# Performance work log

Measured on AMD Instinct MI355X. Metric: run time of the kernel, lower is better.

The kernel has to match this reference:

```python
import jax, jax.numpy as jnp
import numpy as np

# Dimensions (see shape_source): 192x192 images, 10 MC samples, 4 classes (3 fg), batch 16
B, S, CLS, H, W = 16, 10, 4, 192, 192
FG = CLS - 1
FSCALE = 3   # neighbor-count kernel
CSCALE = 3   # constraint-reward kernel
K = float(CSCALE * CSCALE)


def setup_inputs() -> dict:
    key = jax.random.key(0)
    k1, k2 = jax.random.split(key)
    logits = jax.random.normal(k1, (B, CLS, H, W), dtype=jnp.float32)
    preds = jax.nn.softmax(logits, axis=1)          # per-pixel class probabilities
    samples = jax.random.randint(k2, (B, S, H, W), 0, CLS, dtype=jnp.int32)  # sampled label maps
    return {"preds": preds, "samples": samples}


def _conv_ones(x, ksize):
    # x: [N, H, W]; all-ones ksize x ksize conv, SAME padding (== pad (k-1)/2 in torch)
    kern = jnp.ones((1, 1, ksize, ksize), x.dtype)
    y = jax.lax.conv_general_dilated(x[:, None], kern, (1, 1), 'SAME')
    return y[:, 0]


def _dilate8(m):
    # 3x3 max-pool == one step of 8-connectivity dilation (skimage full connectivity)
    return jax.lax.reduce_window(m, 0.0, jax.lax.max, (3, 3), (1, 1), 'SAME')


def _flood(fg, seed):
    # connected component of fg containing flat index `seed` (8-connectivity),
    # equivalent to skimage.flood_fill from the seed followed by == new_value
    m0 = jnp.zeros(fg.size, fg.dtype).at[seed].set(1.0).reshape(fg.shape) * fg
    def cond(st):
        return st[1]
    def body(st):
        m, _ = st
        d = _dilate8(m) * fg
        return d, jnp.any(d != m)
    m, _ = jax.lax.while_loop(cond, body, (m0, jnp.array(True)))
    return m


def _connectivity_rewards(samples):
    # samples: [B, S, H, W] int class maps -> rewards [B, S, H, W]
    cls_ids = jnp.arange(1, CLS)
    fg = (samples[:, :, None] == cls_ids[None, None, :, None, None]).astype(jnp.float32)  # [B,S,FG,H,W]
    fgf = fg.reshape(-1, H, W)                     # [B*S*FG, H, W]
    nb = _conv_ones(fgf, FSCALE) * fgf             # foreground neighbor counts
    seeds = jnp.argmax(nb.reshape(nb.shape[0], -1), axis=1)  # seed = max-neighbor pixel (first max)
    comp = jax.vmap(_flood)(fgf, seeds)            # largest-seeded connected component
    fc = _conv_ones(comp, CSCALE) * comp           # F_fg_neigbors
    reward = fc / K                                # soft reward
    per_c = reward - (fgf - comp)                  # + isolation penalty: -(fg - fill_connect)
    return per_c.reshape(B, S, FG, H, W).sum(axis=2)


def reference(preds, samples):
    rewards = _connectivity_rewards(samples)       # [B,S,H,W], constant wrt preds
    # prob of the sampled class at each pixel: preds[b, samples[b,s,h,w], h, w]
    probs = jnp.take_along_axis(
        jnp.broadcast_to(preds[:, None], (B, S, CLS, H, W)),
        samples[:, :, None].astype(jnp.int32), axis=2)[:, :, 0]
    # REINFORCE-style constraint loss: maximize reward-weighted log-prob
    loss = -(jnp.log(probs + 1e-8) * rewards).mean()
    return loss
```

## Files before the change

kernel.cpp:

```cpp
#include <hip/hip_runtime.h>
#include <stdint.h>

#define BB 16
#define SS 10
#define CLSN 4
#define FGN 3
#define HH 192
#define WW 192
#define NPIX (HH * WW)
#define WPR 3
#define NWORDS (HH * WPR)
#define NPAIR (BB * SS)
#define NTASK (NPAIR * FGN)
#define NT 256
#define NW 4

typedef unsigned long long u64;
typedef unsigned short u16;

#define FAD(a, b, c, s, cy)            \
    do {                               \
        u64 t_ = (a) ^ (b);            \
        (s) = t_ ^ (c);                \
        (cy) = ((a) & (b)) | (t_ & (c)); \
    } while (0)

#define SMEAR3(u0, u1, u2, s0, s1, s2)                          \
    do {                                                        \
        (s0) = (u0) | ((u0) << 1) | ((u0) >> 1) | ((u1) << 63); \
        (s1) = (u1) | ((u1) << 1) | ((u0) >> 63) | ((u1) >> 1) | ((u2) << 63); \
        (s2) = (u2) | ((u2) << 1) | ((u1) >> 63) | ((u2) >> 1); \
    } while (0)

__device__ __forceinline__ void plane9(const u64* bd, int k,
                                       u64& P0, u64& P1, u64& P2, u64& P3, u64& mid)
{
    const int r = k / WPR;
    const int wc = k - r * WPR;
    u64 rows[3][3];
#pragma unroll
    for (int di = 0; di < 3; ++di) {
        int rr = r + di - 1;
#pragma unroll
        for (int dj = 0; dj < 3; ++dj) {
            int ww = wc + dj - 1;
            rows[di][dj] = (rr >= 0 && rr < HH && ww >= 0 && ww < WPR)
                           ? bd[rr * WPR + ww] : 0ULL;
        }
    }
    mid = rows[1][1];
    u64 in[9];
#pragma unroll
    for (int i = 0; i < 3; ++i) {
        u64 m = rows[i][1], lf = rows[i][0], rg = rows[i][2];
        in[3 * i + 0] = m;
        in[3 * i + 1] = (m << 1) | (lf >> 63);
        in[3 * i + 2] = (m >> 1) | (rg << 63);
    }
    u64 s0a, c0a, s0b, c0b, s0c, c0c, c0d, s1a, c1a, c1b;
    FAD(in[0], in[1], in[2], s0a, c0a);
    FAD(in[3], in[4], in[5], s0b, c0b);
    FAD(in[6], in[7], in[8], s0c, c0c);
    FAD(s0a, s0b, s0c, P0, c0d);
    FAD(c0a, c0b, c0c, s1a, c1a);
    P1 = s1a ^ c0d;
    c1b = s1a & c0d;
    P2 = c1a ^ c1b;
    P3 = c1a & c1b;
}

__global__ __launch_bounds__(NT) void cc_fused(
    const float* __restrict__ preds,
    const int* __restrict__ samples,
    double* __restrict__ acc)
{
    __shared__ u64 fgw[NWORDS];
    __shared__ u64 cmp[NWORDS];
    __shared__ unsigned wkey[NW];
    __shared__ double wsum[NW];
    __shared__ unsigned seedSh;
    __shared__ int cntSh;
    __shared__ short wlist[NWORDS];

    const int blk = blockIdx.x;
    const int c = 1 + blk / NPAIR;
    const int pair = blk % NPAIR;
    const int b = pair / SS;

    const int tid  = threadIdx.x;
    const int lane = tid & 63;
    const int wv   = tid >> 6;

    const int* __restrict__ smp  = samples + (size_t)pair * NPIX;
    const float* __restrict__ pp = preds + ((size_t)b * CLSN + c) * NPIX;

    if (tid == 0) cntSh = 0;

    float facc = 0.0f;

    {
        u16* nib = (u16*)fgw;
        for (int sc = 0; sc < 9; ++sc) {
            const int ci = sc * NT + tid;
            const int px = ci << 4;
            const int4 v0 = *(const int4*)(smp + px);
            const int4 v1 = *(const int4*)(smp + px + 4);
            const int4 v2 = *(const int4*)(smp + px + 8);
            const int4 v3 = *(const int4*)(smp + px + 12);
            const float4 q0 = *(const float4*)(pp + px);
            const float4 q1 = *(const float4*)(pp + px + 4);
            const float4 q2 = *(const float4*)(pp + px + 8);
            const float4 q3 = *(const float4*)(pp + px + 12);
            unsigned m = 0u;
#define ACC1(vv, qq, sh)                                              \
            {                                                          \
                const bool hit_ = ((vv) == c);                         \
                m |= ((unsigned)hit_) << (sh);                         \
                facc -= hit_ ? __logf((qq) + 1e-8f) : 0.0f;            \
            }
            ACC1(v0.x, q0.x, 0)  ACC1(v0.y, q0.y, 1)
            ACC1(v0.z, q0.z, 2)  ACC1(v0.w, q0.w, 3)
            ACC1(v1.x, q1.x, 4)  ACC1(v1.y, q1.y, 5)
            ACC1(v1.z, q1.z, 6)  ACC1(v1.w, q1.w, 7)
            ACC1(v2.x, q2.x, 8)  ACC1(v2.y, q2.y, 9)
            ACC1(v2.z, q2.z, 10) ACC1(v2.w, q2.w, 11)
            ACC1(v3.x, q3.x, 12) ACC1(v3.y, q3.y, 13)
            ACC1(v3.z, q3.z, 14) ACC1(v3.w, q3.w, 15)
#undef ACC1
            nib[ci] = (u16)m;
        }
    }
    __syncthreads();

    {
        unsigned bestkey = 0u;
        for (int k = tid; k < NWORDS; k += NT) {
            u64 P0, P1, P2, P3, mid;
            plane9(fgw, k, P0, P1, P2, P3, mid);
            if (mid) {
                u64 cand = mid, t;
                unsigned v = 0;
                t = cand & P3; if (t) { cand = t; v |= 8u; }
                t = cand & P2; if (t) { cand = t; v |= 4u; }
                t = cand & P1; if (t) { cand = t; v |= 2u; }
                t = cand & P0; if (t) { cand = t; v |= 1u; }
                unsigned pix = ((unsigned)k << 6) + (unsigned)(__ffsll(cand) - 1);
                unsigned key = (v << 16) | (36863u - pix);
                if (key > bestkey) bestkey = key;
            }
        }
#pragma unroll
        for (int off = 32; off > 0; off >>= 1) {
            unsigned o = (unsigned)__shfl_xor((int)bestkey, off, 64);
            if (o > bestkey) bestkey = o;
        }
        if (lane == 0) wkey[wv] = bestkey;
    }
    __syncthreads();
    if (tid == 0) {
        unsigned kk = wkey[0];
        if (wkey[1] > kk) kk = wkey[1];
        if (wkey[2] > kk) kk = wkey[2];
        if (wkey[3] > kk) kk = wkey[3];
        seedSh = 36863u - (kk & 0xFFFFu);
    }
    __syncthreads();

    if (wv == 0) {
        const unsigned seed = seedSh;
        u64 f[3][3], cc[3][3];
        const int rbase = 3 * lane;
#pragma unroll
        for (int j = 0; j < 3; ++j)
#pragma unroll
            for (int w = 0; w < 3; ++w) {
                f[j][w] = fgw[(rbase + j) * WPR + w];
                cc[j][w] = 0ULL;
            }
        {
            const int sr = (int)(seed / WW), sw = ((int)seed % WW) >> 6, sb = (int)seed & 63;
            if (sr / 3 == lane)
                cc[sr % 3][sw] = (1ULL << sb) & f[sr % 3][sw];
        }
        for (;;) {
            u64 bA0 = __shfl_up(cc[2][0], 1, 64);
            u64 bA1 = __shfl_up(cc[2][1], 1, 64);
            u64 bA2 = __shfl_up(cc[2][2], 1, 64);
            u64 tB0 = __shfl_down(cc[0][0], 1, 64);
            u64 tB1 = __shfl_down(cc[0][1], 1, 64);
            u64 tB2 = __shfl_down(cc[0][2], 1, 64);
            if (lane == 0)  { bA0 = bA1 = bA2 = 0ULL; }
            if (lane == 63) { tB0 = tB1 = tB2 = 0ULL; }

            u64 o00 = cc[0][0], o01 = cc[0][1], o02 = cc[0][2];
            u64 o10 = cc[1][0], o11 = cc[1][1], o12 = cc[1][2];
            u64 o20 = cc[2][0], o21 = cc[2][1], o22 = cc[2][2];

#define RSTEP(A0, A1, A2, B0, B1, B2, C0, C1, C2, J)                          \
            {                                                                  \
                u64 u0 = (A0) | (B0) | (C0);                                   \
                u64 u1 = (A1) | (B1) | (C1);                                   \
                u64 u2 = (A2) | (B2) | (C2);                                   \
                u64 t0, t1, t2, s0, s1, s2;                                    \
                SMEAR3(u0, u1, u2, t0, t1, t2);                                \
                t0 &= f[J][0]; t1 &= f[J][1]; t2 &= f[J][2];                   \
                SMEAR3(t0, t1, t2, s0, s1, s2);                                \
                cc[J][0] = s0 & f[J][0];                                       \
                cc[J][1] = s1 & f[J][1];                                       \
                cc[J][2] = s2 & f[J][2];                                       \
            }
            RSTEP(bA0, bA1, bA2, cc[0][0], cc[0][1], cc[0][2], cc[1][0], cc[1][1], cc[1][2], 0)
            RSTEP(cc[0][0], cc[0][1], cc[0][2], cc[1][0], cc[1][1], cc[1][2], cc[2][0], cc[2][1], cc[2][2], 1)
            RSTEP(cc[1][0], cc[1][1], cc[1][2], cc[2][0], cc[2][1], cc[2][2], tB0, tB1, tB2, 2)
            RSTEP(cc[0][0], cc[0][1], cc[0][2], cc[1][0], cc[1][1], cc[1][2], cc[2][0], cc[2][1], cc[2][2], 1)
            RSTEP(bA0, bA1, bA2, cc[0][0], cc[0][1], cc[0][2], cc[1][0], cc[1][1], cc[1][2], 0)
#undef RSTEP

            u64 d = (cc[0][0] ^ o00) | (cc[0][1] ^ o01) | (cc[0][2] ^ o02)
                  | (cc[1][0] ^ o10) | (cc[1][1] ^ o11) | (cc[1][2] ^ o12)
                  | (cc[2][0] ^ o20) | (cc[2][1] ^ o21) | (cc[2][2] ^ o22);
            if (!__any(d != 0ULL)) break;
        }
#pragma unroll
        for (int j = 0; j < 3; ++j)
#pragma unroll
            for (int w = 0; w < 3; ++w)
                cmp[(rbase + j) * WPR + w] = cc[j][w];
    }
    __syncthreads();

    for (int k = tid; k < NWORDS; k += NT)
        if (cmp[k] != 0ULL) { int idx = atomicAdd(&cntSh, 1); wlist[idx] = (short)k; }
    __syncthreads();
    {
        const int n = cntSh;
        int i = wv;
        int kc = (i < n) ? (int)wlist[i] : -1;
        float pc = 0.0f;
        if (kc >= 0) pc = pp[(kc << 6) + lane];
        while (kc >= 0) {
            const int i2 = i + NW;
            const int k2 = (i2 < n) ? (int)wlist[i2] : -1;
            float p2 = 0.0f;
            if (k2 >= 0) p2 = pp[(k2 << 6) + lane];
            u64 P0, P1, P2, P3, mid;
            plane9(cmp, kc, P0, P1, P2, P3, mid);
            if ((mid >> lane) & 1ULL) {
                int ct = (int)((P0 >> lane) & 1ULL)
                       | ((int)((P1 >> lane) & 1ULL) << 1)
                       | ((int)((P2 >> lane) & 1ULL) << 2)
                       | ((int)((P3 >> lane) & 1ULL) << 3);
                facc += ((float)ct * (1.0f / 9.0f) + 1.0f) * __logf(pc + 1e-8f);
            }
            i = i2; kc = k2; pc = p2;
        }
    }

#pragma unroll
    for (int off = 32; off > 0; off >>= 1)
        facc += __shfl_xor(facc, off, 64);
    if (lane == 0) wsum[wv] = (double)facc;
    __syncthreads();
    if (tid == 0)
        atomicAdd(acc, wsum[0] + wsum[1] + wsum[2] + wsum[3]);
}

__global__ void finalize_kernel(const double* __restrict__ acc, float* __restrict__ out)
{
    if (threadIdx.x == 0 && blockIdx.x == 0)
        out[0] = (float)(-acc[0] / (double)((long long)BB * SS * NPIX));
}

extern "C" void kernel_launch(void* const* d_in, const int* in_sizes, int n_in,
                              void* d_out, int out_size, void* d_ws, size_t ws_size,
                              hipStream_t stream)
{
    const float* preds   = (const float*)d_in[0];
    const int*   samples = (const int*)d_in[1];
    double* acc = (double*)d_ws;

    hipMemsetAsync(acc, 0, sizeof(double), stream);
    hipLaunchKernelGGL(cc_fused, dim3(NTASK), dim3(NT), 0, stream,
                       preds, samples, acc);
    hipLaunchKernelGGL(finalize_kernel, dim3(1), dim3(64), 0, stream,
                       acc, (float*)d_out);
}
```

Baseline: 49.35 us.

## Flood fill with 8 rows per lane and a forward-backward row sweep

The single-wavefront bitmask flood fill now gives each of 24 active lanes 8 rows instead of giving each of 64 lanes 3 rows. Each iteration sweeps forward and backward over the 8 rows in registers, so information can travel up to 8 rows per iteration instead of 3. The change test is also folded into each step, and the per-row double smear is replaced by a single smear. The aim is fewer iterations of the shuffle-and-vote loop, in exchange for more serial work per lane and higher register pressure, with only 24 of 64 lanes doing useful work.

```diff
diff --git a/kernel.cpp b/kernel.cpp
--- a/kernel.cpp
+++ b/kernel.cpp
@@ -168,64 +168,74 @@
 
     if (wv == 0) {
         const unsigned seed = seedSh;
-        u64 f[3][3], cc[3][3];
-        const int rbase = 3 * lane;
-#pragma unroll
-        for (int j = 0; j < 3; ++j)
+        const bool act = lane < 24;
+        u64 f[8][3], cc[8][3];
+#pragma unroll
+        for (int j = 0; j < 8; ++j)
 #pragma unroll
             for (int w = 0; w < 3; ++w) {
-                f[j][w] = fgw[(rbase + j) * WPR + w];
+                const int k = (8 * lane + j) * WPR + w;
+                f[j][w] = act ? fgw[act ? k : 0] : 0ULL;
                 cc[j][w] = 0ULL;
             }
         {
-            const int sr = (int)(seed / WW), sw = ((int)seed % WW) >> 6, sb = (int)seed & 63;
-            if (sr / 3 == lane)
-                cc[sr % 3][sw] = (1ULL << sb) & f[sr % 3][sw];
+            const int sr = (int)(seed / WW), sc_ = (int)(seed % WW);
+            const int sw = sc_ >> 6, sb = sc_ & 63;
+            if ((sr >> 3) == lane) {
+                const int j = sr & 7;
+                u64 bit = (1ULL << sb);
+#pragma unroll
+                for (int jj = 0; jj < 8; ++jj)
+#pragma unroll
+                    for (int w = 0; w < 3; ++w)
+                        if (jj == j && w == sw) cc[jj][w] = bit & f[jj][w];
+            }
         }
         for (;;) {
-            u64 bA0 = __shfl_up(cc[2][0], 1, 64);
-            u64 bA1 = __shfl_up(cc[2][1], 1, 64);
-            u64 bA2 = __shfl_up(cc[2][2], 1, 64);
+            u64 bA0 = __shfl_up(cc[7][0], 1, 64);
+            u64 bA1 = __shfl_up(cc[7][1], 1, 64);
+            u64 bA2 = __shfl_up(cc[7][2], 1, 64);
             u64 tB0 = __shfl_down(cc[0][0], 1, 64);
             u64 tB1 = __shfl_down(cc[0][1], 1, 64);
             u64 tB2 = __shfl_down(cc[0][2], 1, 64);
-            if (lane == 0)  { bA0 = bA1 = bA2 = 0ULL; }
-            if (lane == 63) { tB0 = tB1 = tB2 = 0ULL; }
-
-            u64 o00 = cc[0][0], o01 = cc[0][1], o02 = cc[0][2];
-            u64 o10 = cc[1][0], o11 = cc[1][1], o12 = cc[1][2];
-            u64 o20 = cc[2][0], o21 = cc[2][1], o22 = cc[2][2];
-
-#define RSTEP(A0, A1, A2, B0, B1, B2, C0, C1, C2, J)                          \
+            if (lane == 0)   { bA0 = bA1 = bA2 = 0ULL; }
+            if (lane >= 23)  { tB0 = tB1 = tB2 = 0ULL; }
+
+            u64 d = 0ULL;
+#define FSTEP(J, T0, T1, T2, B0, B1, B2)                                      \
             {                                                                  \
-                u64 u0 = (A0) | (B0) | (C0);                                   \
-                u64 u1 = (A1) | (B1) | (C1);                                   \
-                u64 u2 = (A2) | (B2) | (C2);                                   \
-                u64 t0, t1, t2, s0, s1, s2;                                    \
-                SMEAR3(u0, u1, u2, t0, t1, t2);                                \
-                t0 &= f[J][0]; t1 &= f[J][1]; t2 &= f[J][2];                   \
-                SMEAR3(t0, t1, t2, s0, s1, s2);                                \
-                cc[J][0] = s0 & f[J][0];                                       \
-                cc[J][1] = s1 & f[J][1];                                       \
-                cc[J][2] = s2 & f[J][2];                                       \
-            }
-            RSTEP(bA0, bA1, bA2, cc[0][0], cc[0][1], cc[0][2], cc[1][0], cc[1][1], cc[1][2], 0)
-            RSTEP(cc[0][0], cc[0][1], cc[0][2], cc[1][0], cc[1][1], cc[1][2], cc[2][0], cc[2][1], cc[2][2], 1)
-            RSTEP(cc[1][0], cc[1][1], cc[1][2], cc[2][0], cc[2][1], cc[2][2], tB0, tB1, tB2, 2)
-            RSTEP(cc[0][0], cc[0][1], cc[0][2], cc[1][0], cc[1][1], cc[1][2], cc[2][0], cc[2][1], cc[2][2], 1)
-            RSTEP(bA0, bA1, bA2, cc[0][0], cc[0][1], cc[0][2], cc[1][0], cc[1][1], cc[1][2], 0)
-#undef RSTEP
-
-            u64 d = (cc[0][0] ^ o00) | (cc[0][1] ^ o01) | (cc[0][2] ^ o02)
-                  | (cc[1][0] ^ o10) | (cc[1][1] ^ o11) | (cc[1][2] ^ o12)
-                  | (cc[2][0] ^ o20) | (cc[2][1] ^ o21) | (cc[2][2] ^ o22);
+                u64 u0 = (T0) | cc[J][0] | (B0);                               \
+                u64 u1 = (T1) | cc[J][1] | (B1);                               \
+                u64 u2 = (T2) | cc[J][2] | (B2);                               \
+                u64 s0, s1, s2;                                                \
+                SMEAR3(u0, u1, u2, s0, s1, s2);                                \
+                s0 &= f[J][0]; s1 &= f[J][1]; s2 &= f[J][2];                   \
+                d |= (s0 & ~cc[J][0]) | (s1 & ~cc[J][1]) | (s2 & ~cc[J][2]);   \
+                cc[J][0] = s0; cc[J][1] = s1; cc[J][2] = s2;                   \
+            }
+            FSTEP(0, bA0, bA1, bA2, cc[1][0], cc[1][1], cc[1][2])
+            FSTEP(1, cc[0][0], cc[0][1], cc[0][2], cc[2][0], cc[2][1], cc[2][2])
+            FSTEP(2, cc[1][0], cc[1][1], cc[1][2], cc[3][0], cc[3][1], cc[3][2])
+            FSTEP(3, cc[2][0], cc[2][1], cc[2][2], cc[4][0], cc[4][1], cc[4][2])
+            FSTEP(4, cc[3][0], cc[3][1], cc[3][2], cc[5][0], cc[5][1], cc[5][2])
+            FSTEP(5, cc[4][0], cc[4][1], cc[4][2], cc[6][0], cc[6][1], cc[6][2])
+            FSTEP(6, cc[5][0], cc[5][1], cc[5][2], cc[7][0], cc[7][1], cc[7][2])
+            FSTEP(7, cc[6][0], cc[6][1], cc[6][2], tB0, tB1, tB2)
+            FSTEP(6, cc[5][0], cc[5][1], cc[5][2], cc[7][0], cc[7][1], cc[7][2])
+            FSTEP(5, cc[4][0], cc[4][1], cc[4][2], cc[6][0], cc[6][1], cc[6][2])
+            FSTEP(4, cc[3][0], cc[3][1], cc[3][2], cc[5][0], cc[5][1], cc[5][2])
+            FSTEP(3, cc[2][0], cc[2][1], cc[2][2], cc[4][0], cc[4][1], cc[4][2])
+            FSTEP(2, cc[1][0], cc[1][1], cc[1][2], cc[3][0], cc[3][1], cc[3][2])
+            FSTEP(1, cc[0][0], cc[0][1], cc[0][2], cc[2][0], cc[2][1], cc[2][2])
+            FSTEP(0, bA0, bA1, bA2, cc[1][0], cc[1][1], cc[1][2])
+#undef FSTEP
             if (!__any(d != 0ULL)) break;
         }
 #pragma unroll
-        for (int j = 0; j < 3; ++j)
+        for (int j = 0; j < 8; ++j)
 #pragma unroll
             for (int w = 0; w < 3; ++w)
-                cmp[(rbase + j) * WPR + w] = cc[j][w];
+                if (act) cmp[(8 * lane + j) * WPR + w] = cc[j][w];
     }
     __syncthreads();
 
```

After: 52.00 us. +5.4%, slower.

## Replace iterative bitmask flood fill with run-length union-find labeling

Applied to the files above, without the earlier changes.

Replaces the single-wave iterative dilation flood fill, whose iteration count grows with component diameter, with run-length encoding of each row, a prefix scan for run offsets, and a block-wide union-find over runs linked to overlapping runs in adjacent rows. Runs whose root matches the seed's run are written back to the component bitmask with atomicOr. This spreads the connectivity work across all 256 threads. In exchange it needs about 74 KB of dynamic shared memory per block, which lowers occupancy, and it adds shared-memory atomics. Runs beyond MAXRUNS are silently dropped.

```diff
diff --git a/kernel.cpp b/kernel.cpp
--- a/kernel.cpp
+++ b/kernel.cpp
@@ -14,22 +14,19 @@
 #define NTASK (NPAIR * FGN)
 #define NT 256
 #define NW 4
+#define MAXRUNS 8192
 
 typedef unsigned long long u64;
 typedef unsigned short u16;
+typedef unsigned int u32;
+
+#define SMEM_BYTES 75536
 
 #define FAD(a, b, c, s, cy)            \
     do {                               \
         u64 t_ = (a) ^ (b);            \
         (s) = t_ ^ (c);                \
         (cy) = ((a) & (b)) | (t_ & (c)); \
-    } while (0)
-
-#define SMEAR3(u0, u1, u2, s0, s1, s2)                          \
-    do {                                                        \
-        (s0) = (u0) | ((u0) << 1) | ((u0) >> 1) | ((u1) << 63); \
-        (s1) = (u1) | ((u1) << 1) | ((u0) >> 63) | ((u1) >> 1) | ((u2) << 63); \
-        (s2) = (u2) | ((u2) << 1) | ((u1) >> 63) | ((u2) >> 1); \
     } while (0)
 
 __device__ __forceinline__ void plane9(const u64* bd, int k,
@@ -69,17 +66,67 @@
     P3 = c1a & c1b;
 }
 
+__device__ __forceinline__ void rowStarts(const u64* fr, u64 st[3])
+{
+    st[0] = fr[0] & ~(fr[0] << 1);
+    st[1] = fr[1] & ~((fr[1] << 1) | (fr[0] >> 63));
+    st[2] = fr[2] & ~((fr[2] << 1) | (fr[1] >> 63));
+}
+
+__device__ __forceinline__ int rankLE(const u64 st[3], int pos)
+{
+    int cnt = 0;
+#pragma unroll
+    for (int w = 0; w < 3; ++w) {
+        const int lo = w << 6;
+        if (pos >= lo + 63) cnt += (int)__popcll(st[w]);
+        else if (pos >= lo) cnt += (int)__popcll(st[w] & ((2ULL << (pos - lo)) - 1ULL));
+    }
+    return cnt;
+}
+
+__device__ __forceinline__ u32 repr(u32 v, u32* P)
+{
+    u32 cur = ((volatile u32*)P)[v];
+    if (cur != v) {
+        u32 prev = v, next;
+        while (cur > (next = ((volatile u32*)P)[cur])) {
+            ((volatile u32*)P)[prev] = next;
+            prev = cur; cur = next;
+        }
+    }
+    return cur;
+}
+
+__device__ __forceinline__ void unite(u32 a, u32 b, u32* P)
+{
+    u32 x = repr(a, P), y = repr(b, P);
+    while (x != y) {
+        if (x < y) { u32 t = x; x = y; y = t; }
+        u32 old = atomicCAS(&P[x], x, y);
+        if (old == x) return;
+        x = repr(old, P);
+        y = repr(y, P);
+    }
+}
+
 __global__ __launch_bounds__(NT) void cc_fused(
     const float* __restrict__ preds,
     const int* __restrict__ samples,
     double* __restrict__ acc)
 {
-    __shared__ u64 fgw[NWORDS];
-    __shared__ u64 cmp[NWORDS];
+    extern __shared__ char smem[];
+    u64* fgw    = (u64*)(smem);
+    u64* cmp    = (u64*)(smem + 4608);
+    u32* runs   = (u32*)(smem + 9216);
+    u32* parent = (u32*)(smem + 41984);
+    int* roff   = (int*)(smem + 74752);
+
     __shared__ unsigned wkey[NW];
     __shared__ double wsum[NW];
     __shared__ unsigned seedSh;
     __shared__ int cntSh;
+    __shared__ u32 seedRunSh;
     __shared__ short wlist[NWORDS];
 
     const int blk = blockIdx.x;
@@ -94,7 +141,7 @@
     const int* __restrict__ smp  = samples + (size_t)pair * NPIX;
     const float* __restrict__ pp = preds + ((size_t)b * CLSN + c) * NPIX;
 
-    if (tid == 0) cntSh = 0;
+    if (tid == 0) { cntSh = 0; seedRunSh = 0xFFFFFFFFu; }
 
     float facc = 0.0f;
 
@@ -166,66 +213,123 @@
     }
     __syncthreads();
 
+    const unsigned seed = seedSh;
+    const int srow = (int)(seed / WW);
+    const int scol = (int)(seed % WW);
+
+    if (tid < HH) {
+        u64 st[3]; rowStarts(fgw + tid * WPR, st);
+        roff[tid] = (int)__popcll(st[0]) + (int)__popcll(st[1]) + (int)__popcll(st[2]);
+    }
+    for (int k = tid; k < NWORDS; k += NT) cmp[k] = 0ULL;
+    __syncthreads();
+
     if (wv == 0) {
-        const unsigned seed = seedSh;
-        u64 f[3][3], cc[3][3];
-        const int rbase = 3 * lane;
-#pragma unroll
-        for (int j = 0; j < 3; ++j)
-#pragma unroll
-            for (int w = 0; w < 3; ++w) {
-                f[j][w] = fgw[(rbase + j) * WPR + w];
-                cc[j][w] = 0ULL;
-            }
-        {
-            const int sr = (int)(seed / WW), sw = ((int)seed % WW) >> 6, sb = (int)seed & 63;
-            if (sr / 3 == lane)
-                cc[sr % 3][sw] = (1ULL << sb) & f[sr % 3][sw];
-        }
-        for (;;) {
-            u64 bA0 = __shfl_up(cc[2][0], 1, 64);
-            u64 bA1 = __shfl_up(cc[2][1], 1, 64);
-            u64 bA2 = __shfl_up(cc[2][2], 1, 64);
-            u64 tB0 = __shfl_down(cc[0][0], 1, 64);
-            u64 tB1 = __shfl_down(cc[0][1], 1, 64);
-            u64 tB2 = __shfl_down(cc[0][2], 1, 64);
-            if (lane == 0)  { bA0 = bA1 = bA2 = 0ULL; }
-            if (lane == 63) { tB0 = tB1 = tB2 = 0ULL; }
-
-            u64 o00 = cc[0][0], o01 = cc[0][1], o02 = cc[0][2];
-            u64 o10 = cc[1][0], o11 = cc[1][1], o12 = cc[1][2];
-            u64 o20 = cc[2][0], o21 = cc[2][1], o22 = cc[2][2];
-
-#define RSTEP(A0, A1, A2, B0, B1, B2, C0, C1, C2, J)                          \
-            {                                                                  \
-                u64 u0 = (A0) | (B0) | (C0);                                   \
-                u64 u1 = (A1) | (B1) | (C1);                                   \
-                u64 u2 = (A2) | (B2) | (C2);                                   \
-                u64 t0, t1, t2, s0, s1, s2;                                    \
-                SMEAR3(u0, u1, u2, t0, t1, t2);                                \
-                t0 &= f[J][0]; t1 &= f[J][1]; t2 &= f[J][2];                   \
-                SMEAR3(t0, t1, t2, s0, s1, s2);                                \
-                cc[J][0] = s0 & f[J][0];                                       \
-                cc[J][1] = s1 & f[J][1];                                       \
-                cc[J][2] = s2 & f[J][2];                                       \
-            }
-            RSTEP(bA0, bA1, bA2, cc[0][0], cc[0][1], cc[0][2], cc[1][0], cc[1][1], cc[1][2], 0)
-            RSTEP(cc[0][0], cc[0][1], cc[0][2], cc[1][0], cc[1][1], cc[1][2], cc[2][0], cc[2][1], cc[2][2], 1)
-            RSTEP(cc[1][0], cc[1][1], cc[1][2], cc[2][0], cc[2][1], cc[2][2], tB0, tB1, tB2, 2)
-            RSTEP(cc[0][0], cc[0][1], cc[0][2], cc[1][0], cc[1][1], cc[1][2], cc[2][0], cc[2][1], cc[2][2], 1)
-            RSTEP(bA0, bA1, bA2, cc[0][0], cc[0][1], cc[0][2], cc[1][0], cc[1][1], cc[1][2], 0)
-#undef RSTEP
-
-            u64 d = (cc[0][0] ^ o00) | (cc[0][1] ^ o01) | (cc[0][2] ^ o02)
-                  | (cc[1][0] ^ o10) | (cc[1][1] ^ o11) | (cc[1][2] ^ o12)
-                  | (cc[2][0] ^ o20) | (cc[2][1] ^ o21) | (cc[2][2] ^ o22);
-            if (!__any(d != 0ULL)) break;
-        }
-#pragma unroll
-        for (int j = 0; j < 3; ++j)
-#pragma unroll
-            for (int w = 0; w < 3; ++w)
-                cmp[(rbase + j) * WPR + w] = cc[j][w];
+        const int r0 = 3 * lane;
+        const int c0 = roff[r0], c1 = roff[r0 + 1], c2 = roff[r0 + 2];
+        int x = c0 + c1 + c2;
+        const int mysum = x;
+#pragma unroll
+        for (int off = 1; off < 64; off <<= 1) {
+            int t = __shfl_up(x, off, 64);
+            if (lane >= off) x += t;
+        }
+        const int excl = x - mysum;
+        roff[r0] = excl;
+        roff[r0 + 1] = excl + c0;
+        roff[r0 + 2] = excl + c0 + c1;
+        if (lane == 63) roff[HH] = x;
+    }
+    __syncthreads();
+
+    if (tid < HH) {
+        const int r = tid;
+        const u64* fr = fgw + r * WPR;
+        u64 st[3]; rowStarts(fr, st);
+        int idx = roff[r];
+#pragma unroll
+        for (int w = 0; w < 3; ++w) {
+            u64 m = st[w];
+            while (m && idx < MAXRUNS) {
+                const int s = (w << 6) + (int)(__ffsll(m) - 1);
+                m &= m - 1;
+                int e = 191;
+                int wj = s >> 6;
+                const int bj = s & 63;
+                u64 inv = ~fr[wj] & (bj == 63 ? 0ULL : (~0ULL << (bj + 1)));
+                while (!inv && wj < 2) { ++wj; inv = ~fr[wj]; }
+                if (inv) e = (wj << 6) + (int)(__ffsll(inv) - 1) - 1;
+                runs[idx] = ((u32)r << 16) | ((u32)s << 8) | (u32)e;
+                parent[idx] = (u32)idx;
+                if (r == srow && s <= scol && scol <= e) seedRunSh = (u32)idx;
+                ++idx;
+            }
+        }
+    }
+    __syncthreads();
+
+    {
+        const int total = roff[HH] < MAXRUNS ? roff[HH] : MAXRUNS;
+        for (int g = tid; g < total; g += NT) {
+            const u32 pk = runs[g];
+            const int r = (int)(pk >> 16);
+            const int s = (int)((pk >> 8) & 0xFFu);
+            const int e = (int)(pk & 0xFFu);
+            const int hi = (e + 1 > 191) ? 191 : e + 1;
+            if (r > 0) {
+                u64 st[3]; rowStarts(fgw + (r - 1) * WPR, st);
+                const int cnt = rankLE(st, hi);
+                if (cnt > 0) {
+                    const int idx = roff[r - 1] + cnt - 1;
+                    if ((int)(runs[idx] & 0xFFu) >= s - 1)
+                        unite((u32)g, (u32)idx, parent);
+                }
+            }
+            if (r < HH - 1) {
+                u64 st[3]; rowStarts(fgw + (r + 1) * WPR, st);
+                const int cnt = rankLE(st, hi);
+                if (cnt > 0) {
+                    const int idx = roff[r + 1] + cnt - 1;
+                    if ((int)(runs[idx] & 0xFFu) >= s - 1)
+                        unite((u32)g, (u32)idx, parent);
+                }
+            }
+        }
+    }
+    __syncthreads();
+
+    {
+        const int total = roff[HH] < MAXRUNS ? roff[HH] : MAXRUNS;
+        for (int g = tid; g < total; g += NT)
+            parent[g] = repr((u32)g, parent);
+    }
+    __syncthreads();
+
+    {
+        const u32 sr = seedRunSh;
+        if (sr != 0xFFFFFFFFu) {
+            const u32 root = parent[sr];
+            const int total = roff[HH] < MAXRUNS ? roff[HH] : MAXRUNS;
+            for (int g = tid; g < total; g += NT) {
+                if (parent[g] == root) {
+                    const u32 pk = runs[g];
+                    const int r = (int)(pk >> 16);
+                    const int s = (int)((pk >> 8) & 0xFFu);
+                    const int e = (int)(pk & 0xFFu);
+#pragma unroll
+                    for (int w = 0; w < 3; ++w) {
+                        const int lo = w << 6;
+                        const int a = s - lo, bq = e - lo;
+                        if (bq < 0 || a > 63) continue;
+                        const int aa = a < 0 ? 0 : a;
+                        const int bb = bq > 63 ? 63 : bq;
+                        const u64 mm = (bb == 63 ? ~0ULL : ((1ULL << (bb + 1)) - 1ULL))
+                                     & (~0ULL << aa);
+                        atomicOr(&cmp[r * WPR + w], mm);
+                    }
+                }
+            }
+        }
     }
     __syncthreads();
 
@@ -280,7 +384,7 @@
     double* acc = (double*)d_ws;
 
     hipMemsetAsync(acc, 0, sizeof(double), stream);
-    hipLaunchKernelGGL(cc_fused, dim3(NTASK), dim3(NT), 0, stream,
+    hipLaunchKernelGGL(cc_fused, dim3(NTASK), dim3(NT), SMEM_BYTES, stream,
                        preds, samples, acc);
     hipLaunchKernelGGL(finalize_kernel, dim3(1), dim3(64), 0, stream,
                        acc, (float*)d_out);
```

Result: slower. 106.1 us (+114.9%).

## Use carry-propagation run fill for horizontal flood propagation within rows

Applied to the files above, without the earlier changes.

Replaces the fixed one-pixel horizontal smear in each flood row-step with a carry-propagation run fill, using addition in both directions through bit reversal. Each row's reached set now extends across whole horizontal foreground runs in a single step. Only vertical and diagonal propagation stays one step per iteration. The goal is fewer wavefront iterations of the shuffle-based flood loop, paid for with more ALU work per step (64-bit adds, brevs and carry compares). The seed is also indexed through static register selection and pre-filled along its row.

```diff
diff --git a/kernel.cpp b/kernel.cpp
--- a/kernel.cpp
+++ b/kernel.cpp
@@ -67,6 +67,35 @@
     c1b = s1a & c0d;
     P2 = c1a ^ c1b;
     P3 = c1a & c1b;
+}
+
+__device__ __forceinline__ void runfill3(const u64 f0, const u64 f1, const u64 f2,
+                                         u64 c0, u64 c1, u64 c2,
+                                         u64& o0, u64& o1, u64& o2)
+{
+    c0 &= f0; c1 &= f1; c2 &= f2;
+    u64 a0 = f0 + c0;  u64 k0 = (u64)(a0 < f0);
+    u64 t1 = f1 + c1;  u64 k1 = (u64)(t1 < f1);
+    u64 a1 = t1 + k0;  k1 |= (u64)(a1 < t1);
+    u64 t2 = f2 + c2;
+    u64 a2 = t2 + k1;
+    const u64 mU0 = a0 & ~f0, mU1 = a1 & ~f1, mU2 = a2 & ~f2;
+    const u64 rf0 = __brevll(f2), rf1 = __brevll(f1), rf2 = __brevll(f0);
+    const u64 rc0 = __brevll(c2), rc1 = __brevll(c1), rc2 = __brevll(c0);
+    u64 b0 = rf0 + rc0; u64 j0 = (u64)(b0 < rf0);
+    u64 u1 = rf1 + rc1; u64 j1 = (u64)(u1 < rf1);
+    u64 b1 = u1 + j0;   j1 |= (u64)(b1 < u1);
+    u64 u2 = rf2 + rc2; u64 j2 = (u64)(u2 < rf2);
+    u64 b2 = u2 + j1;   j2 |= (u64)(b2 < u2);
+    const u64 mD0 = __brevll(b2 & ~rf2);
+    const u64 mD1 = __brevll(b1 & ~rf1);
+    const u64 mD2 = __brevll(b0 & ~rf0);
+    u64 s0 = mU0 - mD0; u64 w0 = (u64)(mU0 < mD0);
+    u64 d0 = s0 - j2;   w0 |= (u64)(s0 < j2);
+    u64 s1 = mU1 - mD1; u64 w1 = (u64)(mU1 < mD1);
+    u64 d1 = s1 - w0;   w1 |= (u64)(s1 < w0);
+    u64 d2 = (mU2 - mD2) - w1;
+    o0 = d0 & f0; o1 = d1 & f1; o2 = d2 & f2;
 }
 
 __global__ __launch_bounds__(NT) void cc_fused(
@@ -178,9 +207,24 @@
                 cc[j][w] = 0ULL;
             }
         {
-            const int sr = (int)(seed / WW), sw = ((int)seed % WW) >> 6, sb = (int)seed & 63;
-            if (sr / 3 == lane)
-                cc[sr % 3][sw] = (1ULL << sb) & f[sr % 3][sw];
+            const int sr = (int)(seed / WW), sc_ = (int)(seed % WW);
+            const int sw = sc_ >> 6, sb = sc_ & 63;
+            if (sr / 3 == lane) {
+                const int jj = sr % 3;
+                u64 bit = (1ULL << sb);
+#pragma unroll
+                for (int j = 0; j < 3; ++j)
+#pragma unroll
+                    for (int w = 0; w < 3; ++w)
+                        if (j == jj && w == sw) cc[j][w] = bit & f[j][w];
+            }
+            if (sr / 3 == lane) {
+                const int jj = sr % 3;
+                u64 n0, n1, n2;
+                runfill3(f[jj][0], f[jj][1], f[jj][2],
+                         cc[jj][0], cc[jj][1], cc[jj][2], n0, n1, n2);
+                cc[jj][0] = n0; cc[jj][1] = n1; cc[jj][2] = n2;
+            }
         }
         for (;;) {
             u64 bA0 = __shfl_up(cc[2][0], 1, 64);
@@ -192,33 +236,24 @@
             if (lane == 0)  { bA0 = bA1 = bA2 = 0ULL; }
             if (lane == 63) { tB0 = tB1 = tB2 = 0ULL; }
 
-            u64 o00 = cc[0][0], o01 = cc[0][1], o02 = cc[0][2];
-            u64 o10 = cc[1][0], o11 = cc[1][1], o12 = cc[1][2];
-            u64 o20 = cc[2][0], o21 = cc[2][1], o22 = cc[2][2];
-
-#define RSTEP(A0, A1, A2, B0, B1, B2, C0, C1, C2, J)                          \
+            u64 d = 0ULL;
+#define RSTEP(J, T0, T1, T2, B0, B1, B2)                                       \
             {                                                                  \
-                u64 u0 = (A0) | (B0) | (C0);                                   \
-                u64 u1 = (A1) | (B1) | (C1);                                   \
-                u64 u2 = (A2) | (B2) | (C2);                                   \
-                u64 t0, t1, t2, s0, s1, s2;                                    \
-                SMEAR3(u0, u1, u2, t0, t1, t2);                                \
-                t0 &= f[J][0]; t1 &= f[J][1]; t2 &= f[J][2];                   \
-                SMEAR3(t0, t1, t2, s0, s1, s2);                                \
-                cc[J][0] = s0 & f[J][0];                                       \
-                cc[J][1] = s1 & f[J][1];                                       \
-                cc[J][2] = s2 & f[J][2];                                       \
-            }
-            RSTEP(bA0, bA1, bA2, cc[0][0], cc[0][1], cc[0][2], cc[1][0], cc[1][1], cc[1][2], 0)
-            RSTEP(cc[0][0], cc[0][1], cc[0][2], cc[1][0], cc[1][1], cc[1][2], cc[2][0], cc[2][1], cc[2][2], 1)
-            RSTEP(cc[1][0], cc[1][1], cc[1][2], cc[2][0], cc[2][1], cc[2][2], tB0, tB1, tB2, 2)
-            RSTEP(cc[0][0], cc[0][1], cc[0][2], cc[1][0], cc[1][1], cc[1][2], cc[2][0], cc[2][1], cc[2][2], 1)
-            RSTEP(bA0, bA1, bA2, cc[0][0], cc[0][1], cc[0][2], cc[1][0], cc[1][1], cc[1][2], 0)
+                u64 v0 = (T0) | (B0), v1 = (T1) | (B1), v2 = (T2) | (B2);      \
+                u64 e0, e1, e2;                                                \
+                SMEAR3(v0, v1, v2, e0, e1, e2);                                \
+                e0 |= cc[J][0]; e1 |= cc[J][1]; e2 |= cc[J][2];                \
+                u64 n0, n1, n2;                                                \
+                runfill3(f[J][0], f[J][1], f[J][2], e0, e1, e2, n0, n1, n2);   \
+                d |= (n0 & ~cc[J][0]) | (n1 & ~cc[J][1]) | (n2 & ~cc[J][2]);   \
+                cc[J][0] = n0; cc[J][1] = n1; cc[J][2] = n2;                   \
+            }
+            RSTEP(0, bA0, bA1, bA2, cc[1][0], cc[1][1], cc[1][2])
+            RSTEP(1, cc[0][0], cc[0][1], cc[0][2], cc[2][0], cc[2][1], cc[2][2])
+            RSTEP(2, cc[1][0], cc[1][1], cc[1][2], tB0, tB1, tB2)
+            RSTEP(1, cc[0][0], cc[0][1], cc[0][2], cc[2][0], cc[2][1], cc[2][2])
+            RSTEP(0, bA0, bA1, bA2, cc[1][0], cc[1][1], cc[1][2])
 #undef RSTEP
-
-            u64 d = (cc[0][0] ^ o00) | (cc[0][1] ^ o01) | (cc[0][2] ^ o02)
-                  | (cc[1][0] ^ o10) | (cc[1][1] ^ o11) | (cc[1][2] ^ o12)
-                  | (cc[2][0] ^ o20) | (cc[2][1] ^ o21) | (cc[2][2] ^ o22);
             if (!__any(d != 0ULL)) break;
         }
 #pragma unroll
```

New measurement: 58.23 us. +18.0%, slower.
